# Optimization experiments

Measured on AMD Instinct MI355X. Metric: run time of the kernel, lower is better.

The kernel has to match this reference:

```python
import jax, jax.numpy as jnp
import numpy as np

N_HEADS = 16
D_HEAD = 64


def setup_inputs() -> dict:
    key = jax.random.key(0)
    ks = jax.random.split(key, 9)
    B, n, L, Lt = 2, 8, 4096, 77
    d, ctx = 1024, 768
    H = W = 64
    s = 0.02  # weight init scale for numerical sanity
    return {
        "x": jax.random.normal(ks[0], (B, L, d), jnp.float32),
        "reorg_masks": jax.random.uniform(ks[1], (B, n, H, W), jnp.float32),
        "text_feat": jax.random.normal(ks[2], (B, n, Lt, ctx), jnp.float32),
        "Wq": jax.random.normal(ks[3], (d, d), jnp.float32) * s,
        "Wk": jax.random.normal(ks[4], (ctx, d), jnp.float32) * s,
        "Wv": jax.random.normal(ks[5], (ctx, d), jnp.float32) * s,
        "Wo": jax.random.normal(ks[6], (d, d), jnp.float32) * s,
        "bo": jax.random.normal(ks[7], (d,), jnp.float32) * s,
        "null_text_feat": jax.random.normal(ks[8], (d,), jnp.float32) * s,
    }


def _cross_attention(xf, ctx, Wq, Wk, Wv, Wo, bo):
    # xf: (BN, L, d), ctx: (BN, Lt, c)
    BN, L, _ = xf.shape
    Lt = ctx.shape[1]
    q = (xf @ Wq).reshape(BN, L, N_HEADS, D_HEAD)
    k = (ctx @ Wk).reshape(BN, Lt, N_HEADS, D_HEAD)
    v = (ctx @ Wv).reshape(BN, Lt, N_HEADS, D_HEAD)
    scale = 1.0 / np.sqrt(D_HEAD).astype(np.float32)
    logits = jnp.einsum("blhd,bthd->bhlt", q, k) * scale
    attn = jax.nn.softmax(logits, axis=-1)
    out = jnp.einsum("bhlt,bthd->blhd", attn, v).reshape(BN, L, N_HEADS * D_HEAD)
    return out @ Wo + bo


def reference(x, reorg_masks, text_feat, Wq, Wk, Wv, Wo, bo, null_text_feat):
    B, L, d = x.shape
    n = reorg_masks.shape[1]
    # masks are already at (H, W) with H*W == L, so nearest interp is identity
    x_flat = jnp.broadcast_to(x[:, None], (B, n, L, d)).reshape(B * n, L, d)
    ctx_flat = text_feat.reshape(B * n, text_feat.shape[2], text_feat.shape[3])
    x_obj = _cross_attention(x_flat, ctx_flat, Wq, Wk, Wv, Wo, bo)
    x_obj = x_obj.reshape(B, n, L, d)
    region = jnp.where(reorg_masks > 0.5, 1.0, 0.0).astype(x.dtype)
    region = region.reshape(B, n, L, 1)  # (b, n, h*w, 1)
    x_sum = jnp.sum(x_obj * region, axis=1)  # (B, L, d)
    cover = jnp.sum(region, axis=1)  # (B, L, 1)
    x_null = (1.0 - cover) * null_text_feat[None, None, :]
    return x_sum + x_null + x
```

## Files before the change

### kernel.cpp

```cpp
#include <hip/hip_runtime.h>


typedef __bf16 bf16;
typedef __bf16 bf16x8 __attribute__((ext_vector_type(8)));
typedef __bf16 bf16x4 __attribute__((ext_vector_type(4)));
typedef float  f32x4  __attribute__((ext_vector_type(4)));

#define MFMA16(a, b, c) __builtin_amdgcn_mfma_f32_16x16x32_bf16((a), (b), (c), 0, 0, 0)


__device__ inline bf16x8 cvt8(const float* p) {
  f32x4 a = *(const f32x4*)p;
  f32x4 b = *(const f32x4*)(p + 4);
  bf16x8 r;
  r[0] = (bf16)a[0]; r[1] = (bf16)a[1]; r[2] = (bf16)a[2]; r[3] = (bf16)a[3];
  r[4] = (bf16)b[0]; r[5] = (bf16)b[1]; r[6] = (bf16)b[2]; r[7] = (bf16)b[3];
  return r;
}

__device__ __forceinline__ void gload_lds16(const bf16* g, bf16* l) {
  __builtin_amdgcn_global_load_lds(
      (const __attribute__((address_space(1))) void*)g,
      (__attribute__((address_space(3))) void*)l, 16, 0, 0);
}

__global__ __launch_bounds__(256) void transpose_all(
    const float* __restrict__ Wq, const float* __restrict__ Wk,
    const float* __restrict__ Wv, const float* __restrict__ Wo,
    bf16* __restrict__ WqT, bf16* __restrict__ WkT,
    bf16* __restrict__ WvT, bf16* __restrict__ WoT,
    const float* __restrict__ mask, float* __restrict__ cover,
    const float* __restrict__ x, bf16* __restrict__ xb) {
  __shared__ bf16 tile[32][33];
  int bx = blockIdx.x;
  int byg = blockIdx.y;
  if (byg == 112) {
    int tid = bx * 256 + threadIdx.x;
    int b = tid >> 12, l = tid & 4095;
    float c = 0.f;
#pragma unroll
    for (int n = 0; n < 8; n++)
      c += (mask[(size_t)(b * 8 + n) * 4096 + l] > 0.5f) ? 1.f : 0.f;
    cover[tid] = c;
    return;
  }
  if (byg >= 113) {
    int gy = byg - 113;
    const size_t blk = (size_t)(gy * 32 + bx) * 1024;
#pragma unroll
    for (int i = 0; i < 4; i++) {
      size_t e = (blk + i * 256 + threadIdx.x) * 8;
      *(bf16x8*)(xb + e) = cvt8(x + e);
    }
    return;
  }
  int tx = threadIdx.x & 31, ty = threadIdx.x >> 5;
  const float* in;
  bf16* out;
  int R, by;
  if (byg < 32)      { in = Wq; out = WqT; R = 1024; by = byg; }
  else if (byg < 56) { in = Wk; out = WkT; R = 768;  by = byg - 32; }
  else if (byg < 80) { in = Wv; out = WvT; R = 768;  by = byg - 56; }
  else               { in = Wo; out = WoT; R = 1024; by = byg - 80; }
  const int C = 1024;
  int c = bx * 32 + tx;
#pragma unroll
  for (int i = 0; i < 32; i += 8) {
    int r = by * 32 + ty + i;
    tile[ty + i][tx] = (bf16)in[(size_t)r * C + c];
  }
  __syncthreads();
#pragma unroll
  for (int i = 0; i < 32; i += 8) {
    out[(size_t)(bx * 32 + ty + i) * R + by * 32 + tx] = tile[tx][ty + i];
  }
}

__device__ __forceinline__ void gemm_q_body(const bf16* __restrict__ Ab,
                                            const bf16* __restrict__ BT,
                                            bf16* __restrict__ C,
                                            int bxn, int bym) {
  __shared__ __align__(16) bf16 sA[2][128 * 32];
  __shared__ __align__(16) bf16 sB[2][128 * 32];
  const int tid = threadIdx.x;
  const int lane = tid & 63, wave = tid >> 6;
  const int l16 = lane & 15, quad = lane >> 4;
  const int m0 = bym * 128, n0 = bxn * 128;
  const int wm = (wave & 1) * 64, wn = (wave >> 1) * 64;

  const int c0 = tid, c1 = 256 + tid;
  const int ar0 = c0 >> 2, ac0 = (c0 & 3) * 8;
  const int ar1 = c1 >> 2, ac1 = (c1 & 3) * 8;
  const int lo0 = (wave * 64) * 8;
  const int lo1 = (256 + wave * 64) * 8;

  const bf16* Arow0 = Ab + (size_t)(m0 + ar0) * 1024 + ac0;
  const bf16* Arow1 = Ab + (size_t)(m0 + ar1) * 1024 + ac1;
  const bf16* Brow0 = BT + (size_t)(n0 + ar0) * 1024 + ac0;
  const bf16* Brow1 = BT + (size_t)(n0 + ar1) * 1024 + ac1;

  gload_lds16(Arow0, &sA[0][lo0]);
  gload_lds16(Arow1, &sA[0][lo1]);
  gload_lds16(Brow0, &sB[0][lo0]);
  gload_lds16(Brow1, &sB[0][lo1]);

  f32x4 acc[4][4];
#pragma unroll
  for (int i = 0; i < 4; i++)
#pragma unroll
    for (int j = 0; j < 4; j++)
#pragma unroll
      for (int r = 0; r < 4; r++) acc[i][j][r] = 0.f;

  __syncthreads();

  int cur = 0;
  for (int kt = 0; kt < 32; kt++) {
    if (kt + 1 < 32) {
      const int nb = cur ^ 1, ko = (kt + 1) * 32;
      gload_lds16(Arow0 + ko, &sA[nb][lo0]);
      gload_lds16(Arow1 + ko, &sA[nb][lo1]);
      gload_lds16(Brow0 + ko, &sB[nb][lo0]);
      gload_lds16(Brow1 + ko, &sB[nb][lo1]);
    }
    bf16x8 a[4], b[4];
#pragma unroll
    for (int mi = 0; mi < 4; mi++)
      a[mi] = *(const bf16x8*)(&sA[cur][(wm + mi * 16 + l16) * 32 + quad * 8]);
#pragma unroll
    for (int ni = 0; ni < 4; ni++)
      b[ni] = *(const bf16x8*)(&sB[cur][(wn + ni * 16 + l16) * 32 + quad * 8]);
#pragma unroll
    for (int mi = 0; mi < 4; mi++)
#pragma unroll
      for (int ni = 0; ni < 4; ni++) acc[mi][ni] = MFMA16(a[mi], b[ni], acc[mi][ni]);
    __syncthreads();
    cur ^= 1;
  }

#pragma unroll
  for (int mi = 0; mi < 4; mi++)
#pragma unroll
    for (int r = 0; r < 4; r++) {
      int row = m0 + wm + mi * 16 + quad * 4 + r;
#pragma unroll
      for (int ni = 0; ni < 4; ni++)
        C[(size_t)row * 1024 + n0 + wn + ni * 16 + l16] = (bf16)(acc[mi][ni][r] * 0.125f);
    }
}

__device__ __forceinline__ void gemm_k_body(const float* __restrict__ text,
                                            const bf16* __restrict__ WkT,
                                            bf16* __restrict__ Kp,
                                            int bx, int bn) {
  const int tid = threadIdx.x;
  const int lane = tid & 63, wave = tid >> 6;
  const int l16 = lane & 15, quad = lane >> 4;
  const int m0 = (wave >> 1) * 64;
  const int n0 = bx * 128 + (wave & 1) * 64;
  const float* A = text + (size_t)bn * 77 * 768;
  bf16* dst = Kp + (size_t)bn * 80 * 1024;

  f32x4 acc[4][4];
#pragma unroll
  for (int i = 0; i < 4; i++)
#pragma unroll
    for (int j = 0; j < 4; j++)
#pragma unroll
      for (int r = 0; r < 4; r++) acc[i][j][r] = 0.f;

  for (int k0 = 0; k0 < 768; k0 += 32) {
    bf16x8 a[4], b[4];
#pragma unroll
    for (int mi = 0; mi < 4; mi++) {
      int row = m0 + mi * 16 + l16;
      if (row >= 77) row = 76;
      a[mi] = cvt8(A + (size_t)row * 768 + k0 + quad * 8);
    }
#pragma unroll
    for (int ni = 0; ni < 4; ni++)
      b[ni] = *(const bf16x8*)(WkT + (size_t)(n0 + ni * 16 + l16) * 768 + k0 + quad * 8);
#pragma unroll
    for (int mi = 0; mi < 4; mi++)
#pragma unroll
      for (int ni = 0; ni < 4; ni++) acc[mi][ni] = MFMA16(a[mi], b[ni], acc[mi][ni]);
  }

#pragma unroll
  for (int mi = 0; mi < 4; mi++)
#pragma unroll
    for (int r = 0; r < 4; r++) {
      int t = m0 + mi * 16 + quad * 4 + r;
      if (t < 77) {
#pragma unroll
        for (int ni = 0; ni < 4; ni++)
          dst[(size_t)t * 1024 + n0 + ni * 16 + l16] = (bf16)acc[mi][ni][r];
      } else if (t < 80) {
#pragma unroll
        for (int ni = 0; ni < 4; ni++)
          dst[(size_t)t * 1024 + n0 + ni * 16 + l16] = (bf16)0.f;
      }
    }
}

__device__ __forceinline__ void gemm_v_body(const float* __restrict__ text,
                                            const bf16* __restrict__ WvT,
                                            bf16* __restrict__ Vt,
                                            int bx, int bn) {
  const int tid = threadIdx.x;
  const int lane = tid & 63, wave = tid >> 6;
  const int l16 = lane & 15, quad = lane >> 4;
  const int m0 = (wave >> 1) * 64;
  const int n0 = bx * 128 + (wave & 1) * 64;
  const float* A = text + (size_t)bn * 77 * 768;
  bf16* dst = Vt + (size_t)bn * 1024 * 96;

  f32x4 acc[4][4];
#pragma unroll
  for (int i = 0; i < 4; i++)
#pragma unroll
    for (int j = 0; j < 4; j++)
#pragma unroll
      for (int r = 0; r < 4; r++) acc[i][j][r] = 0.f;

  for (int k0 = 0; k0 < 768; k0 += 32) {
    bf16x8 a[4], b[4];
#pragma unroll
    for (int mi = 0; mi < 4; mi++) {
      int row = m0 + mi * 16 + l16;
      if (row >= 77) row = 76;
      a[mi] = cvt8(A + (size_t)row * 768 + k0 + quad * 8);
    }
#pragma unroll
    for (int ni = 0; ni < 4; ni++)
      b[ni] = *(const bf16x8*)(WvT + (size_t)(n0 + ni * 16 + l16) * 768 + k0 + quad * 8);
#pragma unroll
    for (int mi = 0; mi < 4; mi++)
#pragma unroll
      for (int ni = 0; ni < 4; ni++) acc[mi][ni] = MFMA16(a[mi], b[ni], acc[mi][ni]);
  }

#pragma unroll
  for (int mi = 0; mi < 4; mi++) {
    int t0 = m0 + mi * 16 + quad * 4;
#pragma unroll
    for (int ni = 0; ni < 4; ni++) {
      int col = n0 + ni * 16 + l16;
      bf16* cbase = dst + (size_t)col * 96;
      if (t0 + 3 < 77) {
        bf16x4 w;
        w[0] = (bf16)acc[mi][ni][0]; w[1] = (bf16)acc[mi][ni][1];
        w[2] = (bf16)acc[mi][ni][2]; w[3] = (bf16)acc[mi][ni][3];
        *(bf16x4*)(cbase + t0) = w;
      } else {
#pragma unroll
        for (int r = 0; r < 4; r++) {
          int t = t0 + r;
          if (t < 77)      cbase[t] = (bf16)acc[mi][ni][r];
          else if (t < 96) cbase[t] = (bf16)0.f;
        }
      }
    }
  }
}

__global__ __launch_bounds__(256) void proj_qkv(const bf16* __restrict__ xb,
                                                const bf16* __restrict__ WqT,
                                                bf16* __restrict__ Qb,
                                                const float* __restrict__ text,
                                                const bf16* __restrict__ WkT,
                                                const bf16* __restrict__ WvT,
                                                bf16* __restrict__ Kp,
                                                bf16* __restrict__ Vt,
                                                int qcount) {
  const int bid = blockIdx.x;
  if (bid < qcount) {
    gemm_q_body(xb, WqT, Qb, bid >> 6, bid & 63);
  } else {
    const int r = bid - qcount;
    const int bx = r & 7, bn = (r >> 3) & 15, kz = r >> 7;
    if (kz == 0) gemm_k_body(text, WkT, Kp, bx, bn);
    else         gemm_v_body(text, WvT, Vt, bx, bn);
  }
}

__global__ __launch_bounds__(256) void gemm_q_f(const float* __restrict__ A,
                                                const bf16* __restrict__ BT,
                                                float* __restrict__ C) {
  const int tid = threadIdx.x;
  const int lane = tid & 63, wave = tid >> 6;
  const int l16 = lane & 15, quad = lane >> 4;
  const int m0 = blockIdx.y * 64;
  const int n0 = blockIdx.x * 256 + wave * 64;

  f32x4 acc[4][4];
#pragma unroll
  for (int i = 0; i < 4; i++)
#pragma unroll
    for (int j = 0; j < 4; j++)
#pragma unroll
      for (int r = 0; r < 4; r++) acc[i][j][r] = 0.f;

  for (int kt = 0; kt < 32; kt++) {
    bf16x8 a[4], b[4];
#pragma unroll
    for (int mi = 0; mi < 4; mi++)
      a[mi] = cvt8(A + (size_t)(m0 + mi * 16 + l16) * 1024 + kt * 32 + quad * 8);
#pragma unroll
    for (int ni = 0; ni < 4; ni++)
      b[ni] = *(const bf16x8*)(BT + (size_t)(n0 + ni * 16 + l16) * 1024 + kt * 32 + quad * 8);
#pragma unroll
    for (int mi = 0; mi < 4; mi++)
#pragma unroll
      for (int ni = 0; ni < 4; ni++) acc[mi][ni] = MFMA16(a[mi], b[ni], acc[mi][ni]);
  }

#pragma unroll
  for (int mi = 0; mi < 4; mi++)
#pragma unroll
    for (int r = 0; r < 4; r++) {
      int row = m0 + mi * 16 + quad * 4 + r;
#pragma unroll
      for (int ni = 0; ni < 4; ni++)
        C[(size_t)row * 1024 + n0 + ni * 16 + l16] = acc[mi][ni][r] * 0.125f;
    }
}

template <typename OutT, typename InT>
__device__ __forceinline__ void attn_body(const InT* Qsrc, OutT* Odst,
                                          const bf16* __restrict__ Kp,
                                          const bf16* __restrict__ Vt,
                                          const float* __restrict__ mask) {
  __shared__ __align__(16) bf16 kl[80 * 72];
  __shared__ __align__(16) bf16 vl[64 * 104];
  __shared__ __align__(16) bf16 p_lds[4][16 * 104];
  const int tid = threadIdx.x;
  const int lane = tid & 63, wave = tid >> 6;
  const int l16 = lane & 15, quad = lane >> 4;
  const int bid = blockIdx.x;
  const int qg = bid & 31;
  const int h = (bid >> 5) & 15;
  const int b = bid >> 9;
  const int qrow0 = qg * 128 + wave * 32;
  bf16* pl = &p_lds[wave][0];

  for (int i = lane; i < 16 * 16; i += 64) {
    int r = i >> 4, c = 80 + (i & 15);
    pl[r * 104 + c] = (bf16)0.f;
  }

  bf16x8 qf[2][2];
#pragma unroll
  for (int mi = 0; mi < 2; mi++)
#pragma unroll
    for (int ks = 0; ks < 2; ks++) {
      const InT* qp = Qsrc + (size_t)(b * 4096 + qrow0 + mi * 16 + l16) * 1024 +
                      h * 64 + ks * 32 + quad * 8;
      if constexpr (sizeof(InT) == 4) qf[mi][ks] = cvt8((const float*)qp);
      else                            qf[mi][ks] = *(const bf16x8*)qp;
    }

  unsigned rbits[2];
#pragma unroll
  for (int mi = 0; mi < 2; mi++) {
    unsigned m = 0;
#pragma unroll
    for (int n = 0; n < 8; n++)
      if (mask[(size_t)(b * 8 + n) * 4096 + qrow0 + mi * 16 + l16] > 0.5f)
        m |= (1u << n);
    rbits[mi] = m;
  }

  f32x4 oacc[2][4];
#pragma unroll
  for (int mi = 0; mi < 2; mi++)
#pragma unroll
    for (int nt = 0; nt < 4; nt++)
#pragma unroll
      for (int r = 0; r < 4; r++) oacc[mi][nt][r] = 0.f;

  for (int n = 0; n < 8; n++) {
    const int bn = b * 8 + n;
    const bf16* Ksrc = Kp + (size_t)bn * 80 * 1024 + h * 64;
    const bf16* Vsrc = Vt + (size_t)bn * 1024 * 96 + (size_t)h * 64 * 96;

    for (int i = tid; i < 640; i += 256) {
      int row = i >> 3, c8 = (i & 7) * 8;
      *(bf16x8*)(kl + row * 72 + c8) = *(const bf16x8*)(Ksrc + (size_t)row * 1024 + c8);
    }
    for (int i = tid; i < 768; i += 256) {
      int row = i / 12, c8 = (i % 12) * 8;
      *(bf16x8*)(vl + row * 104 + c8) = *(const bf16x8*)(Vsrc + (size_t)row * 96 + c8);
    }
    __syncthreads();

    f32x4 s[2][5];
#pragma unroll
    for (int mi = 0; mi < 2; mi++)
#pragma unroll
      for (int tt = 0; tt < 5; tt++)
#pragma unroll
        for (int r = 0; r < 4; r++) s[mi][tt][r] = 0.f;

#pragma unroll
    for (int tt = 0; tt < 5; tt++) {
      int t = tt * 16 + l16;
      bf16x8 kf0 = *(const bf16x8*)(kl + t * 72 + quad * 8);
      bf16x8 kf1 = *(const bf16x8*)(kl + t * 72 + 32 + quad * 8);
#pragma unroll
      for (int mi = 0; mi < 2; mi++) {
        s[mi][tt] = MFMA16(kf0, qf[mi][0], s[mi][tt]);
        s[mi][tt] = MFMA16(kf1, qf[mi][1], s[mi][tt]);
      }
    }

    bf16x8 pfr[2][3];
#pragma unroll
    for (int mi = 0; mi < 2; mi++) {
      float sum = 0.f;
#pragma unroll
      for (int tt = 0; tt < 5; tt++) {
#pragma unroll
        for (int r = 0; r < 4; r++) {
          float e = __expf(s[mi][tt][r]);
          if (tt == 4 && quad * 4 + r >= 13) e = 0.f;
          s[mi][tt][r] = e;
          sum += e;
        }
      }
      sum += __shfl_xor(sum, 16);
      sum += __shfl_xor(sum, 32);
      float rg = ((rbits[mi] >> n) & 1u) ? 1.f : 0.f;
      float scale = rg / sum;
#pragma unroll
      for (int tt = 0; tt < 5; tt++) {
        bf16x4 w;
#pragma unroll
        for (int r = 0; r < 4; r++) w[r] = (bf16)(s[mi][tt][r] * scale);
        *(bf16x4*)(pl + l16 * 104 + tt * 16 + quad * 4) = w;
      }
#pragma unroll
      for (int ks = 0; ks < 3; ks++)
        pfr[mi][ks] = *(const bf16x8*)(pl + l16 * 104 + ks * 32 + quad * 8);
    }

#pragma unroll
    for (int ks = 0; ks < 3; ks++) {
#pragma unroll
      for (int nt = 0; nt < 4; nt++) {
        bf16x8 vf = *(const bf16x8*)(vl + (nt * 16 + l16) * 104 + ks * 32 + quad * 8);
        oacc[0][nt] = MFMA16(pfr[0][ks], vf, oacc[0][nt]);
        oacc[1][nt] = MFMA16(pfr[1][ks], vf, oacc[1][nt]);
      }
    }
    __syncthreads();
  }

#pragma unroll
  for (int mi = 0; mi < 2; mi++)
#pragma unroll
    for (int r = 0; r < 4; r++) {
      size_t row = (size_t)(b * 4096 + qrow0 + mi * 16 + quad * 4 + r);
#pragma unroll
      for (int nt = 0; nt < 4; nt++)
        Odst[row * 1024 + h * 64 + nt * 16 + l16] = (OutT)oacc[mi][nt][r];
    }
}

__global__ __launch_bounds__(256, 4) void attn_b(const bf16* Qb, bf16* ACCb,
                                                 const bf16* __restrict__ Kp,
                                                 const bf16* __restrict__ Vt,
                                                 const float* __restrict__ mask) {
  attn_body<bf16, bf16>(Qb, ACCb, Kp, Vt, mask);
}
__global__ __launch_bounds__(256, 4) void attn_f(float* QO,
                                                 const bf16* __restrict__ Kp,
                                                 const bf16* __restrict__ Vt,
                                                 const float* __restrict__ mask) {
  attn_body<float, float>(QO, QO, Kp, Vt, mask);
}

__global__ __launch_bounds__(256) void gemm_wo_ep2(const bf16* __restrict__ A,
                                                   const bf16* __restrict__ BT,
                                                   const float* __restrict__ x,
                                                   const float* __restrict__ bo,
                                                   const float* __restrict__ nullf,
                                                   const float* __restrict__ cover,
                                                   float* __restrict__ out) {
  __shared__ __align__(16) bf16 sA[2][128 * 32];
  __shared__ __align__(16) bf16 sB[2][128 * 32];
  const int tid = threadIdx.x;
  const int lane = tid & 63, wave = tid >> 6;
  const int l16 = lane & 15, quad = lane >> 4;
  const int m0 = blockIdx.y * 128, n0 = blockIdx.x * 128;
  const int wm = (wave & 1) * 64, wn = (wave >> 1) * 64;

  const int c0 = tid, c1 = 256 + tid;
  const int ar0 = c0 >> 2, ac0 = (c0 & 3) * 8;
  const int ar1 = c1 >> 2, ac1 = (c1 & 3) * 8;
  const int lo0 = (wave * 64) * 8;
  const int lo1 = (256 + wave * 64) * 8;

  const bf16* Arow0 = A + (size_t)(m0 + ar0) * 1024 + ac0;
  const bf16* Arow1 = A + (size_t)(m0 + ar1) * 1024 + ac1;
  const bf16* Brow0 = BT + (size_t)(n0 + ar0) * 1024 + ac0;
  const bf16* Brow1 = BT + (size_t)(n0 + ar1) * 1024 + ac1;

  gload_lds16(Arow0, &sA[0][lo0]);
  gload_lds16(Arow1, &sA[0][lo1]);
  gload_lds16(Brow0, &sB[0][lo0]);
  gload_lds16(Brow1, &sB[0][lo1]);

  f32x4 acc[4][4];
#pragma unroll
  for (int i = 0; i < 4; i++)
#pragma unroll
    for (int j = 0; j < 4; j++)
#pragma unroll
      for (int r = 0; r < 4; r++) acc[i][j][r] = 0.f;

  __syncthreads();

  int cur = 0;
  for (int kt = 0; kt < 32; kt++) {
    if (kt + 1 < 32) {
      const int nb = cur ^ 1, ko = (kt + 1) * 32;
      gload_lds16(Arow0 + ko, &sA[nb][lo0]);
      gload_lds16(Arow1 + ko, &sA[nb][lo1]);
      gload_lds16(Brow0 + ko, &sB[nb][lo0]);
      gload_lds16(Brow1 + ko, &sB[nb][lo1]);
    }
    bf16x8 a[4], b[4];
#pragma unroll
    for (int mi = 0; mi < 4; mi++)
      a[mi] = *(const bf16x8*)(&sA[cur][(wm + mi * 16 + l16) * 32 + quad * 8]);
#pragma unroll
    for (int ni = 0; ni < 4; ni++)
      b[ni] = *(const bf16x8*)(&sB[cur][(wn + ni * 16 + l16) * 32 + quad * 8]);
#pragma unroll
    for (int mi = 0; mi < 4; mi++)
#pragma unroll
      for (int ni = 0; ni < 4; ni++) acc[mi][ni] = MFMA16(a[mi], b[ni], acc[mi][ni]);
    __syncthreads();
    cur ^= 1;
  }

#pragma unroll
  for (int mi = 0; mi < 4; mi++)
#pragma unroll
    for (int r = 0; r < 4; r++) {
      int row = m0 + wm + mi * 16 + quad * 4 + r;
      float cv = cover[row];
#pragma unroll
      for (int ni = 0; ni < 4; ni++) {
        int col = n0 + wn + ni * 16 + l16;
        float v = acc[mi][ni][r] + cv * bo[col] + (1.f - cv) * nullf[col] +
                  x[(size_t)row * 1024 + col];
        out[(size_t)row * 1024 + col] = v;
      }
    }
}

__global__ __launch_bounds__(512) void gemm_wo_ep(float* QO,
                                                  const bf16* __restrict__ WoT,
                                                  const float* __restrict__ x,
                                                  const float* __restrict__ bo,
                                                  const float* __restrict__ nullf,
                                                  const float* __restrict__ cover) {
  __shared__ __align__(16) bf16 lds_a[32 * 32 * 32];
  const int tid = threadIdx.x;
  const int lane = tid & 63, wv = tid >> 6;
  const int l16 = lane & 15, quad = lane >> 4;
  const int m0 = blockIdx.x * 32;

#pragma unroll
  for (int c = 0; c < 16; c++) {
    int ch = c * 512 + tid;
    int row = ch >> 8;
    int pos4 = (ch & 255) * 4;
    int kt = pos4 >> 5, kin = pos4 & 31;
    f32x4 v = *(const f32x4*)(QO + (size_t)(m0 + row) * 1024 + pos4);
    bf16x4 w;
    w[0] = (bf16)v[0]; w[1] = (bf16)v[1]; w[2] = (bf16)v[2]; w[3] = (bf16)v[3];
    *(bf16x4*)(lds_a + kt * 1024 + row * 32 + kin) = w;
  }
  __syncthreads();

  const int n0 = wv * 128;
  f32x4 acc[2][8];
#pragma unroll
  for (int mi = 0; mi < 2; mi++)
#pragma unroll
    for (int ni = 0; ni < 8; ni++)
#pragma unroll
      for (int r = 0; r < 4; r++) acc[mi][ni][r] = 0.f;

  for (int kt = 0; kt < 32; kt++) {
    bf16x8 a[2];
#pragma unroll
    for (int mi = 0; mi < 2; mi++)
      a[mi] = *(const bf16x8*)(lds_a + kt * 1024 + (mi * 16 + l16) * 32 + quad * 8);
    bf16x8 bfr[8];
#pragma unroll
    for (int ni = 0; ni < 8; ni++)
      bfr[ni] = *(const bf16x8*)(WoT + (size_t)(n0 + ni * 16 + l16) * 1024 + kt * 32 + quad * 8);
#pragma unroll
    for (int mi = 0; mi < 2; mi++)
#pragma unroll
      for (int ni = 0; ni < 8; ni++) acc[mi][ni] = MFMA16(a[mi], bfr[ni], acc[mi][ni]);
  }

#pragma unroll
  for (int mi = 0; mi < 2; mi++)
#pragma unroll
    for (int r = 0; r < 4; r++) {
      int row = m0 + mi * 16 + quad * 4 + r;
      float cv = cover[row];
#pragma unroll
      for (int ni = 0; ni < 8; ni++) {
        int col = n0 + ni * 16 + l16;
        float v = acc[mi][ni][r] + cv * bo[col] + (1.f - cv) * nullf[col] +
                  x[(size_t)row * 1024 + col];
        QO[(size_t)row * 1024 + col] = v;
      }
    }
}

extern "C" void kernel_launch(void* const* d_in, const int* in_sizes, int n_in,
                              void* d_out, int out_size, void* d_ws, size_t ws_size,
                              hipStream_t stream) {
  const float* x     = (const float*)d_in[0];
  const float* masks = (const float*)d_in[1];
  const float* text  = (const float*)d_in[2];
  const float* Wq    = (const float*)d_in[3];
  const float* Wk    = (const float*)d_in[4];
  const float* Wv    = (const float*)d_in[5];
  const float* Wo    = (const float*)d_in[6];
  const float* bo    = (const float*)d_in[7];
  const float* nullf = (const float*)d_in[8];
  float* out = (float*)d_out;

  bf16* ws  = (bf16*)d_ws;
  bf16* WqT = ws;
  bf16* WkT = WqT + 1048576;
  bf16* WvT = WkT + 786432;
  bf16* WoT = WvT + 786432;
  bf16* Kp  = WoT + 1048576;
  bf16* Vt  = Kp + 1310720;
  float* cover = (float*)(Vt + 1572864);
  bf16* ACCb = (bf16*)(cover + 8192);
  const size_t NEEDED = 13139968 + 16777216;

  bf16* Qb = (bf16*)d_out;
  bf16* xb = (bf16*)d_out + 8388608;

  transpose_all<<<dim3(32, 145), 256, 0, stream>>>(Wq, Wk, Wv, Wo, WqT, WkT, WvT, WoT,
                                                   masks, cover, x, xb);

  if (ws_size >= NEEDED) {
    proj_qkv<<<768, 256, 0, stream>>>(xb, WqT, Qb, text, WkT, WvT, Kp, Vt, 512);
    attn_b<<<1024, 256, 0, stream>>>(Qb, ACCb, Kp, Vt, masks);
    gemm_wo_ep2<<<dim3(8, 64), 256, 0, stream>>>(ACCb, WoT, x, bo, nullf, cover, out);
  } else {
    proj_qkv<<<256, 256, 0, stream>>>(xb, WqT, nullptr, text, WkT, WvT, Kp, Vt, 0);
    gemm_q_f<<<dim3(4, 128), 256, 0, stream>>>(x, WqT, out);
    attn_f<<<1024, 256, 0, stream>>>(out, Kp, Vt, masks);
    gemm_wo_ep<<<256, 512, 0, stream>>>(out, WoT, x, bo, nullf, cover);
  }
}
```

Measured before the change: 250.7 us.

## Fuse all stages into one cooperative persistent kernel with grid syncs

```diff
diff --git a/kernel.cpp b/kernel.cpp
--- a/kernel.cpp
+++ b/kernel.cpp
@@ -1,4 +1,7 @@
 #include <hip/hip_runtime.h>
+#include <hip/hip_cooperative_groups.h>
+
+namespace cg = cooperative_groups;
 
 
 typedef __bf16 bf16;
@@ -24,16 +27,14 @@
       (__attribute__((address_space(3))) void*)l, 16, 0, 0);
 }
 
-__global__ __launch_bounds__(256) void transpose_all(
+__device__ __forceinline__ void p0_body(
+    int bx, int byg, bf16 (*tile)[33],
     const float* __restrict__ Wq, const float* __restrict__ Wk,
     const float* __restrict__ Wv, const float* __restrict__ Wo,
     bf16* __restrict__ WqT, bf16* __restrict__ WkT,
     bf16* __restrict__ WvT, bf16* __restrict__ WoT,
     const float* __restrict__ mask, float* __restrict__ cover,
     const float* __restrict__ x, bf16* __restrict__ xb) {
-  __shared__ bf16 tile[32][33];
-  int bx = blockIdx.x;
-  int byg = blockIdx.y;
   if (byg == 112) {
     int tid = bx * 256 + threadIdx.x;
     int b = tid >> 12, l = tid & 4095;
@@ -79,9 +80,8 @@
 __device__ __forceinline__ void gemm_q_body(const bf16* __restrict__ Ab,
                                             const bf16* __restrict__ BT,
                                             bf16* __restrict__ C,
-                                            int bxn, int bym) {
-  __shared__ __align__(16) bf16 sA[2][128 * 32];
-  __shared__ __align__(16) bf16 sB[2][128 * 32];
+                                            int bxn, int bym,
+                                            bf16* sAp, bf16* sBp) {
   const int tid = threadIdx.x;
   const int lane = tid & 63, wave = tid >> 6;
   const int l16 = lane & 15, quad = lane >> 4;
@@ -99,10 +99,10 @@
   const bf16* Brow0 = BT + (size_t)(n0 + ar0) * 1024 + ac0;
   const bf16* Brow1 = BT + (size_t)(n0 + ar1) * 1024 + ac1;
 
-  gload_lds16(Arow0, &sA[0][lo0]);
-  gload_lds16(Arow1, &sA[0][lo1]);
-  gload_lds16(Brow0, &sB[0][lo0]);
-  gload_lds16(Brow1, &sB[0][lo1]);
+  gload_lds16(Arow0, sAp + lo0);
+  gload_lds16(Arow1, sAp + lo1);
+  gload_lds16(Brow0, sBp + lo0);
+  gload_lds16(Brow1, sBp + lo1);
 
   f32x4 acc[4][4];
 #pragma unroll
@@ -118,18 +118,18 @@
   for (int kt = 0; kt < 32; kt++) {
     if (kt + 1 < 32) {
       const int nb = cur ^ 1, ko = (kt + 1) * 32;
-      gload_lds16(Arow0 + ko, &sA[nb][lo0]);
-      gload_lds16(Arow1 + ko, &sA[nb][lo1]);
-      gload_lds16(Brow0 + ko, &sB[nb][lo0]);
-      gload_lds16(Brow1 + ko, &sB[nb][lo1]);
+      gload_lds16(Arow0 + ko, sAp + nb * 4096 + lo0);
+      gload_lds16(Arow1 + ko, sAp + nb * 4096 + lo1);
+      gload_lds16(Brow0 + ko, sBp + nb * 4096 + lo0);
+      gload_lds16(Brow1 + ko, sBp + nb * 4096 + lo1);
     }
     bf16x8 a[4], b[4];
 #pragma unroll
     for (int mi = 0; mi < 4; mi++)
-      a[mi] = *(const bf16x8*)(&sA[cur][(wm + mi * 16 + l16) * 32 + quad * 8]);
+      a[mi] = *(const bf16x8*)(sAp + cur * 4096 + (wm + mi * 16 + l16) * 32 + quad * 8);
 #pragma unroll
     for (int ni = 0; ni < 4; ni++)
-      b[ni] = *(const bf16x8*)(&sB[cur][(wn + ni * 16 + l16) * 32 + quad * 8]);
+      b[ni] = *(const bf16x8*)(sBp + cur * 4096 + (wn + ni * 16 + l16) * 32 + quad * 8);
 #pragma unroll
     for (int mi = 0; mi < 4; mi++)
 #pragma unroll
@@ -264,85 +264,20 @@
   }
 }
 
-__global__ __launch_bounds__(256) void proj_qkv(const bf16* __restrict__ xb,
-                                                const bf16* __restrict__ WqT,
-                                                bf16* __restrict__ Qb,
-                                                const float* __restrict__ text,
-                                                const bf16* __restrict__ WkT,
-                                                const bf16* __restrict__ WvT,
-                                                bf16* __restrict__ Kp,
-                                                bf16* __restrict__ Vt,
-                                                int qcount) {
-  const int bid = blockIdx.x;
-  if (bid < qcount) {
-    gemm_q_body(xb, WqT, Qb, bid >> 6, bid & 63);
-  } else {
-    const int r = bid - qcount;
-    const int bx = r & 7, bn = (r >> 3) & 15, kz = r >> 7;
-    if (kz == 0) gemm_k_body(text, WkT, Kp, bx, bn);
-    else         gemm_v_body(text, WvT, Vt, bx, bn);
-  }
-}
-
-__global__ __launch_bounds__(256) void gemm_q_f(const float* __restrict__ A,
-                                                const bf16* __restrict__ BT,
-                                                float* __restrict__ C) {
-  const int tid = threadIdx.x;
-  const int lane = tid & 63, wave = tid >> 6;
-  const int l16 = lane & 15, quad = lane >> 4;
-  const int m0 = blockIdx.y * 64;
-  const int n0 = blockIdx.x * 256 + wave * 64;
-
-  f32x4 acc[4][4];
-#pragma unroll
-  for (int i = 0; i < 4; i++)
-#pragma unroll
-    for (int j = 0; j < 4; j++)
-#pragma unroll
-      for (int r = 0; r < 4; r++) acc[i][j][r] = 0.f;
-
-  for (int kt = 0; kt < 32; kt++) {
-    bf16x8 a[4], b[4];
-#pragma unroll
-    for (int mi = 0; mi < 4; mi++)
-      a[mi] = cvt8(A + (size_t)(m0 + mi * 16 + l16) * 1024 + kt * 32 + quad * 8);
-#pragma unroll
-    for (int ni = 0; ni < 4; ni++)
-      b[ni] = *(const bf16x8*)(BT + (size_t)(n0 + ni * 16 + l16) * 1024 + kt * 32 + quad * 8);
-#pragma unroll
-    for (int mi = 0; mi < 4; mi++)
-#pragma unroll
-      for (int ni = 0; ni < 4; ni++) acc[mi][ni] = MFMA16(a[mi], b[ni], acc[mi][ni]);
-  }
-
-#pragma unroll
-  for (int mi = 0; mi < 4; mi++)
-#pragma unroll
-    for (int r = 0; r < 4; r++) {
-      int row = m0 + mi * 16 + quad * 4 + r;
-#pragma unroll
-      for (int ni = 0; ni < 4; ni++)
-        C[(size_t)row * 1024 + n0 + ni * 16 + l16] = acc[mi][ni][r] * 0.125f;
-    }
-}
-
 template <typename OutT, typename InT>
 __device__ __forceinline__ void attn_body(const InT* Qsrc, OutT* Odst,
                                           const bf16* __restrict__ Kp,
                                           const bf16* __restrict__ Vt,
-                                          const float* __restrict__ mask) {
-  __shared__ __align__(16) bf16 kl[80 * 72];
-  __shared__ __align__(16) bf16 vl[64 * 104];
-  __shared__ __align__(16) bf16 p_lds[4][16 * 104];
+                                          const float* __restrict__ mask,
+                                          int bid, bf16* kl, bf16* vl, bf16* plb) {
   const int tid = threadIdx.x;
   const int lane = tid & 63, wave = tid >> 6;
   const int l16 = lane & 15, quad = lane >> 4;
-  const int bid = blockIdx.x;
   const int qg = bid & 31;
   const int h = (bid >> 5) & 15;
   const int b = bid >> 9;
   const int qrow0 = qg * 128 + wave * 32;
-  bf16* pl = &p_lds[wave][0];
+  bf16* pl = plb + wave * (16 * 104);
 
   for (int i = lane; i < 16 * 16; i += 64) {
     int r = i >> 4, c = 80 + (i & 15);
@@ -467,17 +402,181 @@
     }
 }
 
+__device__ __forceinline__ void wo_body(const bf16* __restrict__ A,
+                                        const bf16* __restrict__ BT,
+                                        const float* __restrict__ x,
+                                        const float* __restrict__ bo,
+                                        const float* __restrict__ nullf,
+                                        const float* __restrict__ cover,
+                                        float* __restrict__ out,
+                                        int bxn, int bym, bf16* sAp, bf16* sBp) {
+  const int tid = threadIdx.x;
+  const int lane = tid & 63, wave = tid >> 6;
+  const int l16 = lane & 15, quad = lane >> 4;
+  const int m0 = bym * 128, n0 = bxn * 128;
+  const int wm = (wave & 1) * 64, wn = (wave >> 1) * 64;
+
+  const int c0 = tid, c1 = 256 + tid;
+  const int ar0 = c0 >> 2, ac0 = (c0 & 3) * 8;
+  const int ar1 = c1 >> 2, ac1 = (c1 & 3) * 8;
+  const int lo0 = (wave * 64) * 8;
+  const int lo1 = (256 + wave * 64) * 8;
+
+  const bf16* Arow0 = A + (size_t)(m0 + ar0) * 1024 + ac0;
+  const bf16* Arow1 = A + (size_t)(m0 + ar1) * 1024 + ac1;
+  const bf16* Brow0 = BT + (size_t)(n0 + ar0) * 1024 + ac0;
+  const bf16* Brow1 = BT + (size_t)(n0 + ar1) * 1024 + ac1;
+
+  gload_lds16(Arow0, sAp + lo0);
+  gload_lds16(Arow1, sAp + lo1);
+  gload_lds16(Brow0, sBp + lo0);
+  gload_lds16(Brow1, sBp + lo1);
+
+  f32x4 acc[4][4];
+#pragma unroll
+  for (int i = 0; i < 4; i++)
+#pragma unroll
+    for (int j = 0; j < 4; j++)
+#pragma unroll
+      for (int r = 0; r < 4; r++) acc[i][j][r] = 0.f;
+
+  __syncthreads();
+
+  int cur = 0;
+  for (int kt = 0; kt < 32; kt++) {
+    if (kt + 1 < 32) {
+      const int nb = cur ^ 1, ko = (kt + 1) * 32;
+      gload_lds16(Arow0 + ko, sAp + nb * 4096 + lo0);
+      gload_lds16(Arow1 + ko, sAp + nb * 4096 + lo1);
+      gload_lds16(Brow0 + ko, sBp + nb * 4096 + lo0);
+      gload_lds16(Brow1 + ko, sBp + nb * 4096 + lo1);
+    }
+    bf16x8 a[4], b[4];
+#pragma unroll
+    for (int mi = 0; mi < 4; mi++)
+      a[mi] = *(const bf16x8*)(sAp + cur * 4096 + (wm + mi * 16 + l16) * 32 + quad * 8);
+#pragma unroll
+    for (int ni = 0; ni < 4; ni++)
+      b[ni] = *(const bf16x8*)(sBp + cur * 4096 + (wn + ni * 16 + l16) * 32 + quad * 8);
+#pragma unroll
+    for (int mi = 0; mi < 4; mi++)
+#pragma unroll
+      for (int ni = 0; ni < 4; ni++) acc[mi][ni] = MFMA16(a[mi], b[ni], acc[mi][ni]);
+    __syncthreads();
+    cur ^= 1;
+  }
+
+#pragma unroll
+  for (int mi = 0; mi < 4; mi++)
+#pragma unroll
+    for (int r = 0; r < 4; r++) {
+      int row = m0 + wm + mi * 16 + quad * 4 + r;
+      float cv = cover[row];
+#pragma unroll
+      for (int ni = 0; ni < 4; ni++) {
+        int col = n0 + wn + ni * 16 + l16;
+        float v = acc[mi][ni][r] + cv * bo[col] + (1.f - cv) * nullf[col] +
+                  x[(size_t)row * 1024 + col];
+        out[(size_t)row * 1024 + col] = v;
+      }
+    }
+}
+
+__global__ __launch_bounds__(256, 4) void mega(
+    const float* __restrict__ Wq, const float* __restrict__ Wk,
+    const float* __restrict__ Wv, const float* __restrict__ Wo,
+    bf16* __restrict__ WqT, bf16* __restrict__ WkT,
+    bf16* __restrict__ WvT, bf16* __restrict__ WoT,
+    const float* __restrict__ mask, float* __restrict__ cover,
+    const float* __restrict__ x, bf16* __restrict__ xb,
+    const float* __restrict__ text,
+    bf16* __restrict__ Qb, bf16* __restrict__ Kp, bf16* __restrict__ Vt,
+    bf16* __restrict__ ACCb,
+    const float* __restrict__ bo, const float* __restrict__ nullf,
+    float* __restrict__ out) {
+  __shared__ __align__(16) char smem[38144];
+  const int bid = blockIdx.x;
+
+  for (int vb = bid; vb < 4640; vb += 1024) {
+    p0_body(vb & 31, vb >> 5, (bf16(*)[33])smem,
+            Wq, Wk, Wv, Wo, WqT, WkT, WvT, WoT, mask, cover, x, xb);
+    __syncthreads();
+  }
+  cg::this_grid().sync();
+
+  if (bid < 512) {
+    gemm_q_body(xb, WqT, Qb, bid >> 6, bid & 63,
+                (bf16*)smem, (bf16*)(smem + 16384));
+  } else if (bid < 768) {
+    const int r = bid - 512;
+    const int bx = r & 7, bn = (r >> 3) & 15, kz = r >> 7;
+    if (kz == 0) gemm_k_body(text, WkT, Kp, bx, bn);
+    else         gemm_v_body(text, WvT, Vt, bx, bn);
+  }
+  cg::this_grid().sync();
+
+  attn_body<bf16, bf16>(Qb, ACCb, Kp, Vt, mask, bid,
+                        (bf16*)smem, (bf16*)(smem + 11520),
+                        (bf16*)(smem + 24832));
+  cg::this_grid().sync();
+
+  if (bid < 512) {
+    wo_body(ACCb, WoT, x, bo, nullf, cover, out, bid & 7, bid >> 3,
+            (bf16*)smem, (bf16*)(smem + 16384));
+  }
+}
+
+__global__ __launch_bounds__(256) void transpose_all(
+    const float* __restrict__ Wq, const float* __restrict__ Wk,
+    const float* __restrict__ Wv, const float* __restrict__ Wo,
+    bf16* __restrict__ WqT, bf16* __restrict__ WkT,
+    bf16* __restrict__ WvT, bf16* __restrict__ WoT,
+    const float* __restrict__ mask, float* __restrict__ cover,
+    const float* __restrict__ x, bf16* __restrict__ xb) {
+  __shared__ __align__(16) bf16 tile[32][33];
+  p0_body(blockIdx.x, blockIdx.y, tile, Wq, Wk, Wv, Wo, WqT, WkT, WvT, WoT,
+          mask, cover, x, xb);
+}
+
+__global__ __launch_bounds__(256) void proj_qkv(const bf16* __restrict__ xb,
+                                                const bf16* __restrict__ WqT,
+                                                bf16* __restrict__ Qb,
+                                                const float* __restrict__ text,
+                                                const bf16* __restrict__ WkT,
+                                                const bf16* __restrict__ WvT,
+                                                bf16* __restrict__ Kp,
+                                                bf16* __restrict__ Vt,
+                                                int qcount) {
+  __shared__ __align__(16) bf16 sbuf[16384];
+  const int bid = blockIdx.x;
+  if (bid < qcount) {
+    gemm_q_body(xb, WqT, Qb, bid >> 6, bid & 63, sbuf, sbuf + 8192);
+  } else {
+    const int r = bid - qcount;
+    const int bx = r & 7, bn = (r >> 3) & 15, kz = r >> 7;
+    if (kz == 0) gemm_k_body(text, WkT, Kp, bx, bn);
+    else         gemm_v_body(text, WvT, Vt, bx, bn);
+  }
+}
+
 __global__ __launch_bounds__(256, 4) void attn_b(const bf16* Qb, bf16* ACCb,
                                                  const bf16* __restrict__ Kp,
                                                  const bf16* __restrict__ Vt,
                                                  const float* __restrict__ mask) {
-  attn_body<bf16, bf16>(Qb, ACCb, Kp, Vt, mask);
-}
+  __shared__ __align__(16) bf16 kl[80 * 72];
+  __shared__ __align__(16) bf16 vl[64 * 104];
+  __shared__ __align__(16) bf16 plb[4 * 16 * 104];
+  attn_body<bf16, bf16>(Qb, ACCb, Kp, Vt, mask, blockIdx.x, kl, vl, plb);
+}
+
 __global__ __launch_bounds__(256, 4) void attn_f(float* QO,
                                                  const bf16* __restrict__ Kp,
                                                  const bf16* __restrict__ Vt,
                                                  const float* __restrict__ mask) {
-  attn_body<float, float>(QO, QO, Kp, Vt, mask);
+  __shared__ __align__(16) bf16 kl[80 * 72];
+  __shared__ __align__(16) bf16 vl[64 * 104];
+  __shared__ __align__(16) bf16 plb[4 * 16 * 104];
+  attn_body<float, float>(QO, QO, Kp, Vt, mask, blockIdx.x, kl, vl, plb);
 }
 
 __global__ __launch_bounds__(256) void gemm_wo_ep2(const bf16* __restrict__ A,
@@ -487,29 +586,19 @@
                                                    const float* __restrict__ nullf,
                                                    const float* __restrict__ cover,
                                                    float* __restrict__ out) {
-  __shared__ __align__(16) bf16 sA[2][128 * 32];
-  __shared__ __align__(16) bf16 sB[2][128 * 32];
+  __shared__ __align__(16) bf16 sbuf[16384];
+  wo_body(A, BT, x, bo, nullf, cover, out, blockIdx.x, blockIdx.y,
+          sbuf, sbuf + 8192);
+}
+
+__global__ __launch_bounds__(256) void gemm_q_f(const float* __restrict__ A,
+                                                const bf16* __restrict__ BT,
+                                                float* __restrict__ C) {
   const int tid = threadIdx.x;
   const int lane = tid & 63, wave = tid >> 6;
   const int l16 = lane & 15, quad = lane >> 4;
-  const int m0 = blockIdx.y * 128, n0 = blockIdx.x * 128;
-  const int wm = (wave & 1) * 64, wn = (wave >> 1) * 64;
-
-  const int c0 = tid, c1 = 256 + tid;
-  const int ar0 = c0 >> 2, ac0 = (c0 & 3) * 8;
-  const int ar1 = c1 >> 2, ac1 = (c1 & 3) * 8;
-  const int lo0 = (wave * 64) * 8;
-  const int lo1 = (256 + wave * 64) * 8;
-
-  const bf16* Arow0 = A + (size_t)(m0 + ar0) * 1024 + ac0;
-  const bf16* Arow1 = A + (size_t)(m0 + ar1) * 1024 + ac1;
-  const bf16* Brow0 = BT + (size_t)(n0 + ar0) * 1024 + ac0;
-  const bf16* Brow1 = BT + (size_t)(n0 + ar1) * 1024 + ac1;
-
-  gload_lds16(Arow0, &sA[0][lo0]);
-  gload_lds16(Arow1, &sA[0][lo1]);
-  gload_lds16(Brow0, &sB[0][lo0]);
-  gload_lds16(Brow1, &sB[0][lo1]);
+  const int m0 = blockIdx.y * 64;
+  const int n0 = blockIdx.x * 256 + wave * 64;
 
   f32x4 acc[4][4];
 #pragma unroll
@@ -519,45 +608,28 @@
 #pragma unroll
       for (int r = 0; r < 4; r++) acc[i][j][r] = 0.f;
 
-  __syncthreads();
-
-  int cur = 0;
   for (int kt = 0; kt < 32; kt++) {
-    if (kt + 1 < 32) {
-      const int nb = cur ^ 1, ko = (kt + 1) * 32;
-      gload_lds16(Arow0 + ko, &sA[nb][lo0]);
-      gload_lds16(Arow1 + ko, &sA[nb][lo1]);
-      gload_lds16(Brow0 + ko, &sB[nb][lo0]);
-      gload_lds16(Brow1 + ko, &sB[nb][lo1]);
-    }
     bf16x8 a[4], b[4];
 #pragma unroll
     for (int mi = 0; mi < 4; mi++)
-      a[mi] = *(const bf16x8*)(&sA[cur][(wm + mi * 16 + l16) * 32 + quad * 8]);
+      a[mi] = cvt8(A + (size_t)(m0 + mi * 16 + l16) * 1024 + kt * 32 + quad * 8);
 #pragma unroll
     for (int ni = 0; ni < 4; ni++)
-      b[ni] = *(const bf16x8*)(&sB[cur][(wn + ni * 16 + l16) * 32 + quad * 8]);
+      b[ni] = *(const bf16x8*)(BT + (size_t)(n0 + ni * 16 + l16) * 1024 + kt * 32 + quad * 8);
 #pragma unroll
     for (int mi = 0; mi < 4; mi++)
 #pragma unroll
       for (int ni = 0; ni < 4; ni++) acc[mi][ni] = MFMA16(a[mi], b[ni], acc[mi][ni]);
-    __syncthreads();
-    cur ^= 1;
   }
 
 #pragma unroll
   for (int mi = 0; mi < 4; mi++)
 #pragma unroll
     for (int r = 0; r < 4; r++) {
-      int row = m0 + wm + mi * 16 + quad * 4 + r;
-      float cv = cover[row];
-#pragma unroll
-      for (int ni = 0; ni < 4; ni++) {
-        int col = n0 + wn + ni * 16 + l16;
-        float v = acc[mi][ni][r] + cv * bo[col] + (1.f - cv) * nullf[col] +
-                  x[(size_t)row * 1024 + col];
-        out[(size_t)row * 1024 + col] = v;
-      }
+      int row = m0 + mi * 16 + quad * 4 + r;
+#pragma unroll
+      for (int ni = 0; ni < 4; ni++)
+        C[(size_t)row * 1024 + n0 + ni * 16 + l16] = acc[mi][ni][r] * 0.125f;
     }
 }
 
@@ -654,14 +726,25 @@
   bf16* Qb = (bf16*)d_out;
   bf16* xb = (bf16*)d_out + 8388608;
 
-  transpose_all<<<dim3(32, 145), 256, 0, stream>>>(Wq, Wk, Wv, Wo, WqT, WkT, WvT, WoT,
-                                                   masks, cover, x, xb);
-
   if (ws_size >= NEEDED) {
+    void* kargs[] = {
+        (void*)&Wq, (void*)&Wk, (void*)&Wv, (void*)&Wo,
+        (void*)&WqT, (void*)&WkT, (void*)&WvT, (void*)&WoT,
+        (void*)&masks, (void*)&cover, (void*)&x, (void*)&xb,
+        (void*)&text, (void*)&Qb, (void*)&Kp, (void*)&Vt,
+        (void*)&ACCb, (void*)&bo, (void*)&nullf, (void*)&out};
+    hipError_t err = hipLaunchCooperativeKernel(
+        (void*)mega, dim3(1024), dim3(256), kargs, 0, stream);
+    if (err == hipSuccess) return;
+    (void)hipGetLastError();
+    transpose_all<<<dim3(32, 145), 256, 0, stream>>>(Wq, Wk, Wv, Wo, WqT, WkT, WvT,
+                                                     WoT, masks, cover, x, xb);
     proj_qkv<<<768, 256, 0, stream>>>(xb, WqT, Qb, text, WkT, WvT, Kp, Vt, 512);
     attn_b<<<1024, 256, 0, stream>>>(Qb, ACCb, Kp, Vt, masks);
     gemm_wo_ep2<<<dim3(8, 64), 256, 0, stream>>>(ACCb, WoT, x, bo, nullf, cover, out);
   } else {
+    transpose_all<<<dim3(32, 145), 256, 0, stream>>>(Wq, Wk, Wv, Wo, WqT, WkT, WvT,
+                                                     WoT, masks, cover, x, xb);
     proj_qkv<<<256, 256, 0, stream>>>(xb, WqT, nullptr, text, WkT, WvT, Kp, Vt, 0);
     gemm_q_f<<<dim3(4, 128), 256, 0, stream>>>(x, WqT, out);
     attn_f<<<1024, 256, 0, stream>>>(out, Kp, Vt, masks);
```

New measurement: 639.0 us. +154.8%, slower.
